# Kernel optimization log

Measured on AMD Instinct MI355X. Metric: run time of the kernel, lower is better.

The kernel has to match this reference:

```python
import jax, jax.numpy as jnp
import numpy as np


def _linear_interp(t, S):
    """1D linear interpolation along last axis, matching F.interpolate(mode='linear', align_corners=False).
    t: [B, C, L] -> [B, C, S]"""
    L = t.shape[-1]
    src = jnp.clip((jnp.arange(S, dtype=jnp.float32) + 0.5) * (L / S) - 0.5, 0.0, L - 1)
    i0 = jnp.floor(src).astype(jnp.int32)
    i1 = jnp.minimum(i0 + 1, L - 1)
    w = (src - i0.astype(jnp.float32)).astype(t.dtype)
    return t[..., i0] * (1.0 - w) + t[..., i1] * w


def setup_inputs() -> dict:
    key = jax.random.key(0)
    k1, k2, k3, k4 = jax.random.split(key, 4)
    B, C, H, W, L, D = 32, 768, 32, 32, 77, 512
    return {
        "img_feat": jax.random.normal(k1, (B, C, H, W), dtype=jnp.float32),
        "text_feat": jax.random.normal(k2, (B, L, D), dtype=jnp.float32),
        "W_txt": jax.random.normal(k3, (D, C), dtype=jnp.float32) / np.float32(np.sqrt(D)),
        "gamma": jax.random.normal(k4, (1,), dtype=jnp.float32) * 0.1,
    }


def reference(img_feat, text_feat, W_txt, gamma):
    B, C, H, W = img_feat.shape
    S = H * W
    q = img_feat.reshape(B, C, S)                          # [B,C,S]
    # Linear(D->C, bias=False) then transpose(1,2): [B,L,D] -> [B,C,L]
    t = jnp.einsum('bld,dc->bcl', text_feat, W_txt)
    t = _linear_interp(t, S)                               # [B,C,S]
    scale = S ** (-0.5)
    # attn = bmm(q [B,C,S], t^T [B,S,C]) * scale -> [B,C,C] channel attention
    attn = jax.nn.softmax(jnp.einsum('bis,bjs->bij', q, t) * scale, axis=-1)
    out = q + gamma * jnp.einsum('bij,bjs->bis', attn, t)  # gamma-gated residual
    return out.reshape(B, C, H, W)
```

## Files before the change

kernel.cpp:

```cpp
#include <hip/hip_runtime.h>

#define BB 32
#define CC 768
#define SS 1024
#define LLn 77
#define DD 512
#define LP 80
#define LP2 96

#define RATIO 0.0751953125f
#define IRATIO 13.298701f

#define CVT_TXT_BLOCKS (BB * LP * DD / 4 / 256)
#define CVT_W_BLOCKS ((CC / 32) * (DD / 32))
#define TG_BLOCKS (BB * 5 * 4)

typedef short bf16x8 __attribute__((ext_vector_type(8)));
typedef float f32x4 __attribute__((ext_vector_type(4)));
typedef unsigned short u16;

__device__ __forceinline__ float bf2f(unsigned int h16) {
    unsigned int u = h16 << 16;
    float f; __builtin_memcpy(&f, &u, 4); return f;
}
__device__ __forceinline__ u16 f2bf(float f) {
    unsigned int u; __builtin_memcpy(&u, &f, 4);
    u += 0x7fffu + ((u >> 16) & 1u);
    return (u16)(u >> 16);
}

__global__ __launch_bounds__(256) void k_cvt(const float* __restrict__ text,
                                             const float* __restrict__ Wt,
                                             u16* __restrict__ At,
                                             u16* __restrict__ Wb) {
    __shared__ float tile[32 * 33];
    const int bx = blockIdx.x;
    const int tid = threadIdx.x;
    if (bx < CVT_TXT_BLOCKS) {
        int j = bx * 256 + tid;
        int row80 = j >> 7, col4 = (j & 127) << 2;
        int b = row80 / LP, l = row80 - b * LP;
        u16 o[4] = {0, 0, 0, 0};
        if (l < LLn) {
            float4 v = *reinterpret_cast<const float4*>(&text[((size_t)b * LLn + l) * DD + col4]);
            o[0] = f2bf(v.x); o[1] = f2bf(v.y); o[2] = f2bf(v.z); o[3] = f2bf(v.w);
        }
        *reinterpret_cast<uint2*>(&At[(size_t)row80 * DD + col4]) = *reinterpret_cast<uint2*>(o);
    } else {
        const int bw = bx - CVT_TXT_BLOCKS;
        const int c0 = (bw % (CC / 32)) * 32, d0 = (bw / (CC / 32)) * 32;
        const int tx = tid & 31, ty = tid >> 5;
#pragma unroll
        for (int k = 0; k < 4; ++k) {
            int d = ty + k * 8;
            tile[d * 33 + tx] = Wt[(size_t)(d0 + d) * CC + c0 + tx];
        }
        __syncthreads();
#pragma unroll
        for (int k = 0; k < 4; ++k) {
            int c = ty + k * 8;
            Wb[(size_t)(c0 + c) * DD + d0 + tx] = f2bf(tile[tx * 33 + c]);
        }
    }
}

__global__ __launch_bounds__(256) void k_tgemm(const u16* __restrict__ At,
                                               const u16* __restrict__ Wb,
                                               u16* __restrict__ tc,
                                               u16* __restrict__ tlc) {
    const int bx = blockIdx.x;
    const int tid = threadIdx.x;
    const int cg = bx / 160, mt = bx % 160;
    const int b = mt / 5, tile = mt % 5;
    const int l0 = tile * 16;
    const int w = tid >> 6, lane = tid & 63;
    const int lm = lane & 15, lg = lane >> 4;
    const int c0 = cg * 192 + w * 48;

    f32x4 acc[3];
#pragma unroll
    for (int nt = 0; nt < 3; ++nt) acc[nt] = (f32x4){0.f, 0.f, 0.f, 0.f};

    const u16* ap = At + ((size_t)b * LP + l0 + lm) * DD + lg * 8;
    const u16* bp = Wb + (size_t)(c0 + lm) * DD + lg * 8;
#pragma unroll 4
    for (int ks = 0; ks < 16; ++ks) {
        bf16x8 aq = *reinterpret_cast<const bf16x8*>(ap + ks * 32);
#pragma unroll
        for (int nt = 0; nt < 3; ++nt) {
            bf16x8 bv = *reinterpret_cast<const bf16x8*>(bp + (size_t)nt * 16 * DD + ks * 32);
            acc[nt] = __builtin_amdgcn_mfma_f32_16x16x32_bf16(aq, bv, acc[nt], 0, 0, 0);
        }
    }

    const int lq = l0 + lg * 4;
#pragma unroll
    for (int nt = 0; nt < 3; ++nt) {
        int c = c0 + nt * 16 + lm;
        u16 pk[4];
#pragma unroll
        for (int r = 0; r < 4; ++r) pk[r] = f2bf(acc[nt][r]);
        uint2 pv; __builtin_memcpy(&pv, pk, 8);
        *reinterpret_cast<uint2*>(&tc[((size_t)b * CC + c) * LP2 + lq]) = pv;
#pragma unroll
        for (int r = 0; r < 4; ++r)
            tlc[((size_t)b * LP + lq + r) * CC + c] = pk[r];
    }
    if (tile == 4 && lg == 0) {
        uint4 z = {0u, 0u, 0u, 0u};
#pragma unroll
        for (int nt = 0; nt < 3; ++nt) {
            int c = c0 + nt * 16 + lm;
            *reinterpret_cast<uint4*>(&tc[((size_t)b * CC + c) * LP2 + 80]) = z;
            *reinterpret_cast<uint4*>(&tc[((size_t)b * CC + c) * LP2 + 88]) = z;
        }
    }
}

__global__ __launch_bounds__(256, 2) void k_fused(const u16* __restrict__ tc,
                                                  const u16* __restrict__ tlc,
                                                  const float* __restrict__ q,
                                                  const float* __restrict__ gamma,
                                                  float* __restrict__ out) {
    __shared__ __align__(16) char un[32768];
    u16* qlds = (u16*)un;
    char* pbufBase = un;
    float* us = (float*)(un + 25600);
    float* pmax = (float*)(un + 30720);
    float* psum = (float*)(un + 30976);
    __shared__ u16 qh_bf[16 * 96];

    const int b = blockIdx.y;
    const int iBase = blockIdx.x * 16;
    const int tid = threadIdx.x;
    const int w = tid >> 6, lane = tid & 63;
    const int lm = lane & 15, lg = lane >> 4;
    const float g = gamma[0];

    const size_t qBase = ((size_t)b * CC + iBase) * SS + (size_t)(tid << 2);
    f32x4 qreg[16];
#pragma unroll
    for (int r = 0; r < 16; ++r)
        qreg[r] = *reinterpret_cast<const f32x4*>(&q[qBase + (size_t)r * SS]);
    const int s0 = tid << 2;
#pragma unroll
    for (int r = 0; r < 16; ++r) {
        u16 pk[4] = {f2bf(qreg[r][0]), f2bf(qreg[r][1]), f2bf(qreg[r][2]), f2bf(qreg[r][3])};
        uint2 pv; __builtin_memcpy(&pv, pk, 8);
        *reinterpret_cast<uint2*>(&qlds[r * 1024 + s0]) = pv;
    }
    __syncthreads();

#pragma unroll
    for (int k = 0; k < 5; ++k) {
        int e = tid + (k << 8);
        int r = e / 80, l = e - r * 80;
        float val = 0.f;
        if (l < LLn) {
            int slo = max(0, (int)floorf(((float)l - 0.5f) * IRATIO - 0.5f) - 1);
            int shi = min(SS - 1, (int)ceilf(((float)l + 1.5f) * IRATIO - 0.5f) + 1);
            float fl = (float)l;
            float a = 0.f;
            for (int s = slo; s <= shi; ++s) {
                float src = fmaf((float)s + 0.5f, RATIO, -0.5f);
                src = fminf(fmaxf(src, 0.f), 76.f);
                float wgt = fmaxf(0.f, 1.f - fabsf(src - fl));
                a = fmaf(wgt, bf2f(qlds[r * 1024 + s]), a);
            }
            val = a * 0.03125f;
        }
        qh_bf[r * 96 + l] = f2bf(val);
    }
    {
        int i = tid;
        if (i < 16 * 16) qh_bf[(i >> 4) * 96 + 80 + (i & 15)] = 0;
    }
    __syncthreads();

    bf16x8 aq0 = *reinterpret_cast<const bf16x8*>(&qh_bf[lm * 96 + lg * 8]);
    bf16x8 aq1 = *reinterpret_cast<const bf16x8*>(&qh_bf[lm * 96 + 32 + lg * 8]);
    bf16x8 aq2 = *reinterpret_cast<const bf16x8*>(&qh_bf[lm * 96 + 64 + lg * 8]);

    f32x4 acc[12];
#pragma unroll
    for (int t = 0; t < 12; ++t) acc[t] = (f32x4){0.f, 0.f, 0.f, 0.f};

    const u16* tcb = tc + ((size_t)b * CC + w * 192 + lm) * LP2 + lg * 8;
#pragma unroll
    for (int t = 0; t < 12; ++t) {
        const u16* p = tcb + (size_t)t * 16 * LP2;
        bf16x8 b0 = *reinterpret_cast<const bf16x8*>(p);
        bf16x8 b1 = *reinterpret_cast<const bf16x8*>(p + 32);
        bf16x8 b2 = *reinterpret_cast<const bf16x8*>(p + 64);
        acc[t] = __builtin_amdgcn_mfma_f32_16x16x32_bf16(aq0, b0, acc[t], 0, 0, 0);
        acc[t] = __builtin_amdgcn_mfma_f32_16x16x32_bf16(aq1, b1, acc[t], 0, 0, 0);
        acc[t] = __builtin_amdgcn_mfma_f32_16x16x32_bf16(aq2, b2, acc[t], 0, 0, 0);
    }

    float m[4];
#pragma unroll
    for (int r = 0; r < 4; ++r) {
        float mm = acc[0][r];
#pragma unroll
        for (int t = 1; t < 12; ++t) mm = fmaxf(mm, acc[t][r]);
#pragma unroll
        for (int off = 8; off >= 1; off >>= 1) mm = fmaxf(mm, __shfl_xor(mm, off));
        m[r] = mm;
    }
    if (lm == 0) {
#pragma unroll
        for (int r = 0; r < 4; ++r) pmax[w * 16 + lg * 4 + r] = m[r];
    }
    __syncthreads();
    float gm[4];
#pragma unroll
    for (int r = 0; r < 4; ++r) {
        int row = lg * 4 + r;
        gm[r] = fmaxf(fmaxf(pmax[row], pmax[16 + row]), fmaxf(pmax[32 + row], pmax[48 + row]));
    }
    float s[4] = {0.f, 0.f, 0.f, 0.f};
#pragma unroll
    for (int t = 0; t < 12; ++t) {
#pragma unroll
        for (int r = 0; r < 4; ++r) {
            float e = __expf(acc[t][r] - gm[r]);
            acc[t][r] = e;
            s[r] += e;
        }
    }
#pragma unroll
    for (int r = 0; r < 4; ++r) {
#pragma unroll
        for (int off = 8; off >= 1; off >>= 1) s[r] += __shfl_xor(s[r], off);
    }
    if (lm == 0) {
#pragma unroll
        for (int r = 0; r < 4; ++r) psum[w * 16 + lg * 4 + r] = s[r];
    }

    u16* P = (u16*)(pbufBase + w * 6400);
#pragma unroll
    for (int t = 0; t < 12; ++t) {
#pragma unroll
        for (int r = 0; r < 4; ++r)
            P[(lg * 4 + r) * 200 + t * 16 + lm] = f2bf(acc[t][r]);
    }

    f32x4 u[5];
#pragma unroll
    for (int nt = 0; nt < 5; ++nt) u[nt] = (f32x4){0.f, 0.f, 0.f, 0.f};
    const u16* tb = tlc + ((size_t)b * LP + lm) * CC + w * 192 + lg * 8;
#pragma unroll
    for (int ks = 0; ks < 6; ++ks) {
        bf16x8 pa = *reinterpret_cast<const bf16x8*>(&P[lm * 200 + ks * 32 + lg * 8]);
#pragma unroll
        for (int nt = 0; nt < 5; ++nt) {
            bf16x8 bv = *reinterpret_cast<const bf16x8*>(tb + (size_t)nt * 16 * CC + ks * 32);
            u[nt] = __builtin_amdgcn_mfma_f32_16x16x32_bf16(pa, bv, u[nt], 0, 0, 0);
        }
    }

    float* up = (float*)(pbufBase + w * 6400);
#pragma unroll
    for (int nt = 0; nt < 5; ++nt) {
#pragma unroll
        for (int r = 0; r < 4; ++r)
            up[(lg * 4 + r) * 81 + nt * 16 + lm] = u[nt][r];
    }
    __syncthreads();
#pragma unroll
    for (int k = 0; k < 5; ++k) {
        int idx = tid + (k << 8);
        int row = idx / LP, l = idx - row * LP;
        float v = ((float*)(pbufBase))[row * 81 + l]
                + ((float*)(pbufBase + 6400))[row * 81 + l]
                + ((float*)(pbufBase + 12800))[row * 81 + l]
                + ((float*)(pbufBase + 19200))[row * 81 + l];
        float denom = psum[row] + psum[16 + row] + psum[32 + row] + psum[48 + row];
        us[row * LP + l] = v / denom;
    }
    __syncthreads();

    float wgt[4]; int i0k[4], i1x[4];
#pragma unroll
    for (int k = 0; k < 4; ++k) {
        float src = fmaf((float)(s0 + k) + 0.5f, RATIO, -0.5f);
        src = fminf(fmaxf(src, 0.f), 76.f);
        i0k[k] = (int)src;
        wgt[k] = src - (float)i0k[k];
        i1x[k] = (i0k[k] < 76) ? i0k[k] + 1 : 76;
    }
#pragma unroll
    for (int r = 0; r < 16; ++r) {
        const float* ur = &us[r * LP];
        f32x4 o;
#pragma unroll
        for (int k = 0; k < 4; ++k) {
            float uv = fmaf(1.f - wgt[k], ur[i0k[k]], wgt[k] * ur[i1x[k]]);
            o[k] = qreg[r][k] + g * uv;
        }
        __builtin_nontemporal_store(o, reinterpret_cast<f32x4*>(&out[qBase + (size_t)r * SS]));
    }
}

extern "C" void kernel_launch(void* const* d_in, const int* in_sizes, int n_in,
                              void* d_out, int out_size, void* d_ws, size_t ws_size,
                              hipStream_t stream) {
    const float* img   = (const float*)d_in[0];
    const float* text  = (const float*)d_in[1];
    const float* Wt    = (const float*)d_in[2];
    const float* gamma = (const float*)d_in[3];
    float* out = (float*)d_out;
    char* ws = (char*)d_ws;
    u16*   tc_bf  = (u16*)(ws);
    u16*   tlc_bf = (u16*)(ws + 4718592);
    u16*   At_bf  = (u16*)(ws + 8650752);
    u16*   Wb_bf  = (u16*)(ws + 11272192);

    k_cvt<<<dim3(CVT_TXT_BLOCKS + CVT_W_BLOCKS), 256, 0, stream>>>(text, Wt, At_bf, Wb_bf);
    k_tgemm<<<dim3(TG_BLOCKS), 256, 0, stream>>>(At_bf, Wb_bf, tc_bf, tlc_bf);
    k_fused<<<dim3(48, BB), 256, 0, stream>>>(tc_bf, tlc_bf, img, gamma, out);
}
```

Measured before the change: 100.9 us.

## Compute interpolation-adjoint projection of q via MFMA with precomputed weight matrix

The per-thread scalar loop that projects each q row onto the 77 text positions (the adjoint of the linear interpolation) is replaced. A bf16 interpolation weight matrix [80 x 1024] is now built in the conversion kernel, and the projection is done as an MFMA GEMM split across the four waves along S, with partial sums reduced through LDS. The q LDS row stride is padded to avoid bank conflicts on the bf16x8 loads. This trades scalar FMA work for extra global reads of the weight matrix, extra LDS traffic and syncs, and bf16 rounding of the weights.

```diff
diff --git a/kernel.cpp b/kernel.cpp
--- a/kernel.cpp
+++ b/kernel.cpp
@@ -7,22 +7,19 @@
 #define DD 512
 #define LP 80
 #define LP2 96
+#define QSTR 1048
 
 #define RATIO 0.0751953125f
-#define IRATIO 13.298701f
 
 #define CVT_TXT_BLOCKS (BB * LP * DD / 4 / 256)
 #define CVT_W_BLOCKS ((CC / 32) * (DD / 32))
+#define AB_BLOCKS (LP * SS / 4 / 256)
 #define TG_BLOCKS (BB * 5 * 4)
 
 typedef short bf16x8 __attribute__((ext_vector_type(8)));
 typedef float f32x4 __attribute__((ext_vector_type(4)));
 typedef unsigned short u16;
 
-__device__ __forceinline__ float bf2f(unsigned int h16) {
-    unsigned int u = h16 << 16;
-    float f; __builtin_memcpy(&f, &u, 4); return f;
-}
 __device__ __forceinline__ u16 f2bf(float f) {
     unsigned int u; __builtin_memcpy(&u, &f, 4);
     u += 0x7fffu + ((u >> 16) & 1u);
@@ -32,7 +29,8 @@
 __global__ __launch_bounds__(256) void k_cvt(const float* __restrict__ text,
                                              const float* __restrict__ Wt,
                                              u16* __restrict__ At,
-                                             u16* __restrict__ Wb) {
+                                             u16* __restrict__ Wb,
+                                             u16* __restrict__ Ab) {
     __shared__ float tile[32 * 33];
     const int bx = blockIdx.x;
     const int tid = threadIdx.x;
@@ -46,7 +44,7 @@
             o[0] = f2bf(v.x); o[1] = f2bf(v.y); o[2] = f2bf(v.z); o[3] = f2bf(v.w);
         }
         *reinterpret_cast<uint2*>(&At[(size_t)row80 * DD + col4]) = *reinterpret_cast<uint2*>(o);
-    } else {
+    } else if (bx < CVT_TXT_BLOCKS + CVT_W_BLOCKS) {
         const int bw = bx - CVT_TXT_BLOCKS;
         const int c0 = (bw % (CC / 32)) * 32, d0 = (bw / (CC / 32)) * 32;
         const int tx = tid & 31, ty = tid >> 5;
@@ -61,6 +59,20 @@
             int c = ty + k * 8;
             Wb[(size_t)(c0 + c) * DD + d0 + tx] = f2bf(tile[tx * 33 + c]);
         }
+    } else {
+        int i4 = (bx - CVT_TXT_BLOCKS - CVT_W_BLOCKS) * 256 + tid;
+        int l = i4 >> 8;
+        int sc = (i4 & 255) << 2;
+        float fl = (float)l;
+        u16 o[4];
+#pragma unroll
+        for (int k = 0; k < 4; ++k) {
+            float src = fmaf((float)(sc + k) + 0.5f, RATIO, -0.5f);
+            src = fminf(fmaxf(src, 0.f), 76.f);
+            float w = fmaxf(0.f, 1.f - fabsf(src - fl)) * 0.03125f;
+            o[k] = f2bf(w);
+        }
+        *reinterpret_cast<uint2*>(&Ab[(size_t)l * SS + sc]) = *reinterpret_cast<uint2*>(o);
     }
 }
 
@@ -119,10 +131,11 @@
 
 __global__ __launch_bounds__(256, 2) void k_fused(const u16* __restrict__ tc,
                                                   const u16* __restrict__ tlc,
+                                                  const u16* __restrict__ Ab,
                                                   const float* __restrict__ q,
                                                   const float* __restrict__ gamma,
                                                   float* __restrict__ out) {
-    __shared__ __align__(16) char un[32768];
+    __shared__ __align__(16) char un[16 * QSTR * 2];
     u16* qlds = (u16*)un;
     char* pbufBase = un;
     float* us = (float*)(un + 25600);
@@ -147,29 +160,45 @@
     for (int r = 0; r < 16; ++r) {
         u16 pk[4] = {f2bf(qreg[r][0]), f2bf(qreg[r][1]), f2bf(qreg[r][2]), f2bf(qreg[r][3])};
         uint2 pv; __builtin_memcpy(&pv, pk, 8);
-        *reinterpret_cast<uint2*>(&qlds[r * 1024 + s0]) = pv;
-    }
-    __syncthreads();
-
+        *reinterpret_cast<uint2*>(&qlds[r * QSTR + s0]) = pv;
+    }
+    __syncthreads();
+
+    f32x4 aqh[5];
+#pragma unroll
+    for (int nt = 0; nt < 5; ++nt) aqh[nt] = (f32x4){0.f, 0.f, 0.f, 0.f};
+    {
+        const u16* abBase = Ab + (size_t)lm * SS + w * 256 + lg * 8;
+#pragma unroll
+        for (int kk = 0; kk < 8; ++kk) {
+            bf16x8 av = *reinterpret_cast<const bf16x8*>(&qlds[lm * QSTR + w * 256 + kk * 32 + lg * 8]);
+#pragma unroll
+            for (int nt = 0; nt < 5; ++nt) {
+                bf16x8 bv = *reinterpret_cast<const bf16x8*>(abBase + (size_t)nt * 16 * SS + kk * 32);
+                aqh[nt] = __builtin_amdgcn_mfma_f32_16x16x32_bf16(av, bv, aqh[nt], 0, 0, 0);
+            }
+        }
+    }
+    __syncthreads();
+    {
+        float* qp = (float*)(pbufBase + w * 6400);
+#pragma unroll
+        for (int nt = 0; nt < 5; ++nt) {
+#pragma unroll
+            for (int r = 0; r < 4; ++r)
+                qp[(lg * 4 + r) * 80 + nt * 16 + lm] = aqh[nt][r];
+        }
+    }
+    __syncthreads();
 #pragma unroll
     for (int k = 0; k < 5; ++k) {
         int e = tid + (k << 8);
-        int r = e / 80, l = e - r * 80;
-        float val = 0.f;
-        if (l < LLn) {
-            int slo = max(0, (int)floorf(((float)l - 0.5f) * IRATIO - 0.5f) - 1);
-            int shi = min(SS - 1, (int)ceilf(((float)l + 1.5f) * IRATIO - 0.5f) + 1);
-            float fl = (float)l;
-            float a = 0.f;
-            for (int s = slo; s <= shi; ++s) {
-                float src = fmaf((float)s + 0.5f, RATIO, -0.5f);
-                src = fminf(fmaxf(src, 0.f), 76.f);
-                float wgt = fmaxf(0.f, 1.f - fabsf(src - fl));
-                a = fmaf(wgt, bf2f(qlds[r * 1024 + s]), a);
-            }
-            val = a * 0.03125f;
-        }
-        qh_bf[r * 96 + l] = f2bf(val);
+        int row = e / 80, l = e - row * 80;
+        float v = ((float*)(pbufBase))[row * 80 + l]
+                + ((float*)(pbufBase + 6400))[row * 80 + l]
+                + ((float*)(pbufBase + 12800))[row * 80 + l]
+                + ((float*)(pbufBase + 19200))[row * 80 + l];
+        qh_bf[row * 96 + l] = f2bf(v);
     }
     {
         int i = tid;
@@ -316,8 +345,10 @@
     u16*   tlc_bf = (u16*)(ws + 4718592);
     u16*   At_bf  = (u16*)(ws + 8650752);
     u16*   Wb_bf  = (u16*)(ws + 11272192);
-
-    k_cvt<<<dim3(CVT_TXT_BLOCKS + CVT_W_BLOCKS), 256, 0, stream>>>(text, Wt, At_bf, Wb_bf);
+    u16*   Ab_bf  = (u16*)(ws + 12058624);
+
+    k_cvt<<<dim3(CVT_TXT_BLOCKS + CVT_W_BLOCKS + AB_BLOCKS), 256, 0, stream>>>(
+        text, Wt, At_bf, Wb_bf, Ab_bf);
     k_tgemm<<<dim3(TG_BLOCKS), 256, 0, stream>>>(At_bf, Wb_bf, tc_bf, tlc_bf);
-    k_fused<<<dim3(48, BB), 256, 0, stream>>>(tc_bf, tlc_bf, img, gamma, out);
-}
+    k_fused<<<dim3(48, BB), 256, 0, stream>>>(tc_bf, tlc_bf, Ab_bf, img, gamma, out);
+}
```

New measurement: 115.5 us. +14.5%, slower.
